# Performance work log

Measured on AMD Instinct MI355X. Metric: run time of the kernel, lower is better.

## Reference

```python
import jax, jax.numpy as jnp
import numpy as np

NEG_INF = -1e30
EPS = 1e-7  # keras.backend.epsilon()

B, T, C, L = 256, 1024, 128, 128


def setup_inputs() -> dict:
    key = jax.random.key(0)
    k1, k2, k3, k4 = jax.random.split(key, 4)
    # ctc_batch_cost expects softmax probabilities in y_pred
    y_pred = jax.nn.softmax(jax.random.normal(k1, (B, T, C), dtype=jnp.float32), axis=-1)
    y_true = jax.random.randint(k2, (B, L), 0, C - 1)           # blank = C-1 excluded from labels
    input_length = jax.random.randint(k3, (B, 1), T // 2, T + 1)
    label_length = jax.random.randint(k4, (B, 1), L // 2, L + 1)
    return {"y_true": y_true, "y_pred": y_pred,
            "input_length": input_length, "label_length": label_length}


def _ctc_batch_cost(y_true, y_pred, input_length, label_length):
    """Faithful jax version of keras.backend.ctc_batch_cost (blank = num_classes-1)."""
    b, t_max, c = y_pred.shape
    l_max = y_true.shape[1]
    s_max = 2 * l_max + 1
    blank = c - 1

    logp = jnp.log(y_pred + EPS)                                # [B,T,C]

    # Extended label sequence: blank, l0, blank, l1, ..., blank  -> [B,S]
    ext = jnp.full((b, s_max), blank, dtype=y_true.dtype)
    ext = ext.at[:, 1::2].set(y_true)

    # Gather log-probs of extended labels per time step -> [B,T,S]
    lp_ext = jnp.take_along_axis(logp, ext[:, None, :], axis=2)

    # Skip transition (s-2 -> s) allowed iff ext[s] != blank and ext[s] != ext[s-2]
    same = jnp.concatenate([jnp.ones((b, 2), bool), ext[:, 2:] == ext[:, :-2]], axis=1)
    skip_ok = (ext != blank) & (~same)                          # [B,S]

    # Valid extended positions given per-sample label_length
    s_idx = jnp.arange(s_max)
    valid_s = s_idx[None, :] < (2 * label_length + 1)           # [B,S]

    ll = label_length[:, 0]
    il = input_length[:, 0]

    alpha0 = jnp.full((b, s_max), NEG_INF, dtype=logp.dtype)
    alpha0 = alpha0.at[:, 0].set(lp_ext[:, 0, 0])
    alpha0 = alpha0.at[:, 1].set(jnp.where(ll > 0, lp_ext[:, 0, 1], NEG_INF))

    neg1 = jnp.full((b, 1), NEG_INF, dtype=logp.dtype)
    neg2 = jnp.full((b, 2), NEG_INF, dtype=logp.dtype)

    def step(alpha, inputs):
        lp_t, t = inputs                                        # lp_t: [B,S]
        a1 = alpha
        a2 = jnp.concatenate([neg1, alpha[:, :-1]], axis=1)
        a3 = jnp.where(skip_ok, jnp.concatenate([neg2, alpha[:, :-2]], axis=1), NEG_INF)
        m = jnp.maximum(jnp.maximum(a1, a2), a3)
        new = m + jnp.log(jnp.exp(a1 - m) + jnp.exp(a2 - m) + jnp.exp(a3 - m)) + lp_t
        new = jnp.where(valid_s, new, NEG_INF)
        alpha = jnp.where((t < il)[:, None], new, alpha)        # freeze past input_length
        return alpha, None

    lp_seq = jnp.moveaxis(lp_ext, 1, 0)[1:]                     # [T-1,B,S]
    ts = jnp.arange(1, t_max)
    alpha_T, _ = jax.lax.scan(step, alpha0, (lp_seq, ts))

    end = 2 * ll                                                # index of final blank
    a_end = jnp.take_along_axis(alpha_T, end[:, None], axis=1)[:, 0]
    a_pen = jnp.take_along_axis(alpha_T, jnp.maximum(end - 1, 0)[:, None], axis=1)[:, 0]
    a_pen = jnp.where(ll > 0, a_pen, NEG_INF)
    loglik = jnp.logaddexp(a_end, a_pen)
    return -loglik[:, None]                                     # [B,1], as ctc_batch_cost


def reference(y_true, y_pred, input_length, label_length):
    # CTCLayer.call computes the loss (add_loss) and returns y_pred; for the
    # kernel baseline we return the loss itself, which is the actual compute.
    return _ctc_batch_cost(y_true, y_pred, input_length, label_length)
```

## Files before the change

kernel.cpp:

```cpp
#include <hip/hip_runtime.h>


constexpr int   Tn    = 1024;
constexpr int   Cc    = 128;
constexpr int   Ln    = 128;
constexpr float EPSf  = 1e-7f;
constexpr int   CK    = 15;
constexpr int   NSLOT = 4;

__device__ __forceinline__ int dpp_max_i32(int m) {
    int o;
    o = __builtin_amdgcn_update_dpp(0, m, 0x111, 0xf, 0xf, false); m = o > m ? o : m;
    o = __builtin_amdgcn_update_dpp(0, m, 0x112, 0xf, 0xf, false); m = o > m ? o : m;
    o = __builtin_amdgcn_update_dpp(0, m, 0x114, 0xf, 0xf, false); m = o > m ? o : m;
    o = __builtin_amdgcn_update_dpp(0, m, 0x118, 0xf, 0xf, false); m = o > m ? o : m;
    o = __builtin_amdgcn_update_dpp(0, m, 0x142, 0xf, 0xf, false); m = o > m ? o : m;
    o = __builtin_amdgcn_update_dpp(0, m, 0x143, 0xf, 0xf, false); m = o > m ? o : m;
    return m;
}

__device__ __forceinline__ double dpp_shr1_f64(double x) {
    const int lo = __double2loint(x), hi = __double2hiint(x);
    const int slo = __builtin_amdgcn_update_dpp(0, lo, 0x138, 0xf, 0xf, true);
    const int shi = __builtin_amdgcn_update_dpp(0, hi, 0x138, 0xf, 0xf, true);
    return __hiloint2double(shi, slo);
}

__global__ __launch_bounds__(128, 1)
void ctc_fwd_kernel(const int*   __restrict__ y_true,
                    const float* __restrict__ y_pred,
                    const int*   __restrict__ in_len,
                    const int*   __restrict__ lab_len,
                    float*       __restrict__ out)
{
    const int tid = threadIdx.x;
    const int L   = tid & 63;
    const int b   = blockIdx.x;
    const int il  = in_len[b];
    const int ll  = lab_len[b];
    const int blank = Cc - 1;

    const int* yb   = y_true + (size_t)b * Ln;
    const int  lab1 = yb[2 * L];
    const int  lab2 = yb[2 * L + 1];

    const float* base = y_pred + (size_t)b * Tn * Cc;
    const int steps = (il > 0) ? (il - 1) : 0;
    const int nfull = steps / CK;
    const int nch   = (steps + CK - 1) / CK;

    __shared__ float  f32L1[NSLOT][CK][64];
    __shared__ float  f32L2[NSLOT][CK][64];
    __shared__ float  f32BK[NSLOT][CK];
    __shared__ double sA[258];

#define BARRIER() do {                                                  \
    __builtin_amdgcn_sched_barrier(0);                                  \
    asm volatile("" ::: "memory");                                      \
    __builtin_amdgcn_s_barrier();                                       \
    asm volatile("" ::: "memory");                                      \
    __builtin_amdgcn_sched_barrier(0);                                  \
} while (0)

#define WAIT_VM(n) do {                                                 \
    __builtin_amdgcn_sched_barrier(0);                                  \
    asm volatile("s_waitcnt vmcnt(" #n ")");                            \
    __builtin_amdgcn_sched_barrier(0);                                  \
} while (0)

    if (tid >= 64) {
#define ISSUE_CHUNK(k) do {                                             \
    const int slot_ = (k) & (NSLOT - 1);                                \
    {                                                                   \
        int tb_ = 1 + (k) * CK + L; if (tb_ > steps) tb_ = steps; if (tb_ < 0) tb_ = 0; \
        const float* g_ = base + (size_t)tb_ * Cc + blank;              \
        if (L < CK)                                                     \
            __builtin_amdgcn_global_load_lds(                           \
                (const __attribute__((address_space(1))) void*)g_,      \
                (__attribute__((address_space(3))) void*)&f32BK[slot_][0], 4, 0, 0); \
    }                                                                   \
    _Pragma("unroll")                                                   \
    for (int r_ = 0; r_ < CK; ++r_) {                                   \
        int t_ = 1 + (k) * CK + r_; if (t_ > steps) t_ = steps; if (t_ < 0) t_ = 0; \
        const float* row_ = base + (size_t)t_ * Cc;                     \
        __builtin_amdgcn_global_load_lds(                               \
            (const __attribute__((address_space(1))) void*)(row_ + lab1), \
            (__attribute__((address_space(3))) void*)&f32L1[slot_][r_][0], 4, 0, 0); \
        __builtin_amdgcn_global_load_lds(                               \
            (const __attribute__((address_space(1))) void*)(row_ + lab2), \
            (__attribute__((address_space(3))) void*)&f32L2[slot_][r_][0], 4, 0, 0); \
    }                                                                   \
} while (0)

        ISSUE_CHUNK(0);
        ISSUE_CHUNK(1);
        WAIT_VM(31);
        BARRIER();
        for (int i = 0; i < nch; ++i) {
            if (i + 2 < nch) {
                ISSUE_CHUNK(i + 2);
                WAIT_VM(31);
            } else {
                WAIT_VM(0);
            }
            BARRIER();
        }
        return;
#undef ISSUE_CHUNK
    }

    const int  labp = (L > 0) ? yb[2 * L - 1] : -1;
    const double skm1 = ((L > 0) && (lab1 != blank) && (lab1 != labp)) ? 1.0 : 0.0;
    const double skm3 = ((lab2 != blank) && (lab2 != lab1)) ? 1.0 : 0.0;

    double a0 = 0.0, a1v = 0.0, a2v = 0.0, a3v = 0.0, a4v = 0.0;
    if (L == 0) {
        a0  = (double)(base[blank] + EPSf);
        a1v = (ll > 0) ? (double)(base[lab1] + EPSf) : 0.0;
    }
    int shift = 0;

#define DPSTEP(qb_, q1_, q2_) do {                                      \
    const double pa3_ = dpp_shr1_f64(a3v);                              \
    const double n0_ = (a0 + pa3_) * (qb_);                             \
    const double n1_ = fma(skm1, pa3_, a0 + a1v) * (q1_);               \
    const double n2_ = (a2v + a1v) * (qb_);                             \
    const double n3_ = fma(skm3, a1v, a3v + a2v) * (q2_);               \
    const double n4_ = (a4v + a3v) * (qb_);                             \
    a0 = n0_; a1v = n1_; a2v = n2_; a3v = n3_; a4v = n4_;               \
} while (0)

#define RESCALE() do {                                                  \
    double m_ = fmax(fmax(a0, a1v), fmax(a2v, a3v)); m_ = fmax(m_, a4v);\
    int be_ = (__double2hiint(m_) >> 20) & 0x7ff;                       \
    be_ = dpp_max_i32(be_);                                             \
    const int emax_ = __builtin_amdgcn_readlane(be_, 63);               \
    const double sc_ = __hiloint2double((2046 - emax_) << 20, 0);       \
    a0 *= sc_; a1v *= sc_; a2v *= sc_; a3v *= sc_; a4v *= sc_;          \
    shift += emax_ - 1023;                                              \
} while (0)

    BARRIER();

    for (int i = 0; i < nch; ++i) {
        const int slot = i & (NSLOT - 1);

        double qb[CK], q1[CK], q2[CK];
#pragma unroll
        for (int r = 0; r < CK; ++r) {
            qb[r] = (double)(f32BK[slot][r]    + EPSf);
            q1[r] = (double)(f32L1[slot][r][L] + EPSf);
            q2[r] = (double)(f32L2[slot][r][L] + EPSf);
        }

        BARRIER();

        if (i < nfull) {
#pragma unroll
            for (int r = 0; r < CK; ++r)
                DPSTEP(qb[r], q1[r], q2[r]);
        } else {
#pragma unroll
            for (int r = 0; r < CK; ++r) {
                if (1 + i * CK + r <= steps)
                    DPSTEP(qb[r], q1[r], q2[r]);
            }
        }
        RESCALE();
    }

    sA[4 * L + 0] = a0;
    sA[4 * L + 1] = a1v;
    sA[4 * L + 2] = a2v;
    sA[4 * L + 3] = a3v;
    if (L == 63) sA[256] = a4v;

    if (L == 0) {
        const int end = 2 * ll;
        const double ae = sA[end];
        int pi = end - 1; if (pi < 0) pi = 0;
        double ap = sA[pi];
        if (ll <= 0) ap = 0.0;
        const double s  = ae + ap;
        const double lg = log2(s) + (double)shift;
        out[b] = (float)(-0.6931471805599453 * lg);
    }

#undef BARRIER
#undef WAIT_VM
#undef DPSTEP
#undef RESCALE
}

extern "C" void kernel_launch(void* const* d_in, const int* in_sizes, int n_in,
                              void* d_out, int out_size, void* d_ws, size_t ws_size,
                              hipStream_t stream) {
    const int*   y_true  = (const int*)  d_in[0];
    const float* y_pred  = (const float*)d_in[1];
    const int*   in_len  = (const int*)  d_in[2];
    const int*   lab_len = (const int*)  d_in[3];
    float*       out     = (float*)      d_out;

    ctc_fwd_kernel<<<dim3(256), dim3(128), 0, stream>>>(y_true, y_pred, in_len, lab_len, out);
}
```

Before: 58.49 us.

## Switch CTC alpha recursion from fp64 to fp32 with per-lane exponent shifts

Replaces the double-precision scaled-probability recursion with fp32, keeping a separate exponent offset for each lane instead of one wave-wide shift. Neighbour contributions are rescaled with ldexp by the clamped difference in lane shifts, and lanes whose values fall too far below their left neighbour are zeroed. The chunk size drops from 15 to 8 time steps, so fewer values are held in registers but rescaling runs more often. This removes slow fp64 arithmetic, at the cost of more complicated rescale logic and possible accuracy loss.

Result: slower. 70.90 us (+21.2%).

```diff
diff --git a/kernel.cpp b/kernel.cpp
--- a/kernel.cpp
+++ b/kernel.cpp
@@ -5,25 +5,15 @@
 constexpr int   Cc    = 128;
 constexpr int   Ln    = 128;
 constexpr float EPSf  = 1e-7f;
-constexpr int   CK    = 15;
+constexpr int   CK    = 8;
 constexpr int   NSLOT = 4;
 
-__device__ __forceinline__ int dpp_max_i32(int m) {
-    int o;
-    o = __builtin_amdgcn_update_dpp(0, m, 0x111, 0xf, 0xf, false); m = o > m ? o : m;
-    o = __builtin_amdgcn_update_dpp(0, m, 0x112, 0xf, 0xf, false); m = o > m ? o : m;
-    o = __builtin_amdgcn_update_dpp(0, m, 0x114, 0xf, 0xf, false); m = o > m ? o : m;
-    o = __builtin_amdgcn_update_dpp(0, m, 0x118, 0xf, 0xf, false); m = o > m ? o : m;
-    o = __builtin_amdgcn_update_dpp(0, m, 0x142, 0xf, 0xf, false); m = o > m ? o : m;
-    o = __builtin_amdgcn_update_dpp(0, m, 0x143, 0xf, 0xf, false); m = o > m ? o : m;
-    return m;
-}
-
-__device__ __forceinline__ double dpp_shr1_f64(double x) {
-    const int lo = __double2loint(x), hi = __double2hiint(x);
-    const int slo = __builtin_amdgcn_update_dpp(0, lo, 0x138, 0xf, 0xf, true);
-    const int shi = __builtin_amdgcn_update_dpp(0, hi, 0x138, 0xf, 0xf, true);
-    return __hiloint2double(shi, slo);
+__device__ __forceinline__ float dpp_shr1_f32(float x) {
+    int s = __builtin_amdgcn_update_dpp(0, __float_as_int(x), 0x138, 0xf, 0xf, true);
+    return __int_as_float(s);
+}
+__device__ __forceinline__ int dpp_shr1_i32(int x) {
+    return __builtin_amdgcn_update_dpp(0, x, 0x138, 0xf, 0xf, true);
 }
 
 __global__ __launch_bounds__(128, 1)
@@ -49,10 +39,11 @@
     const int nfull = steps / CK;
     const int nch   = (steps + CK - 1) / CK;
 
-    __shared__ float  f32L1[NSLOT][CK][64];
-    __shared__ float  f32L2[NSLOT][CK][64];
-    __shared__ float  f32BK[NSLOT][CK];
-    __shared__ double sA[258];
+    __shared__ float f32L1[NSLOT][CK][64];
+    __shared__ float f32L2[NSLOT][CK][64];
+    __shared__ float f32BK[NSLOT][CK];
+    __shared__ float sAf[258];
+    __shared__ int   sShL[64];
 
 #define BARRIER() do {                                                  \
     __builtin_amdgcn_sched_barrier(0);                                  \
@@ -94,12 +85,12 @@
 
         ISSUE_CHUNK(0);
         ISSUE_CHUNK(1);
-        WAIT_VM(31);
+        WAIT_VM(17);
         BARRIER();
         for (int i = 0; i < nch; ++i) {
             if (i + 2 < nch) {
                 ISSUE_CHUNK(i + 2);
-                WAIT_VM(31);
+                WAIT_VM(17);
             } else {
                 WAIT_VM(0);
             }
@@ -109,35 +100,56 @@
 #undef ISSUE_CHUNK
     }
 
-    const int  labp = (L > 0) ? yb[2 * L - 1] : -1;
-    const double skm1 = ((L > 0) && (lab1 != blank) && (lab1 != labp)) ? 1.0 : 0.0;
-    const double skm3 = ((lab2 != blank) && (lab2 != lab1)) ? 1.0 : 0.0;
-
-    double a0 = 0.0, a1v = 0.0, a2v = 0.0, a3v = 0.0, a4v = 0.0;
+    const int  labp  = (L > 0) ? yb[2 * L - 1] : -1;
+    const float skm1 = ((L > 0) && (lab1 != blank) && (lab1 != labp)) ? 1.0f : 0.0f;
+    const float skm3 = ((lab2 != blank) && (lab2 != lab1)) ? 1.0f : 0.0f;
+
+    float a0 = 0.f, a1v = 0.f, a2v = 0.f, a3v = 0.f, a4v = 0.f;
     if (L == 0) {
-        a0  = (double)(base[blank] + EPSf);
-        a1v = (ll > 0) ? (double)(base[lab1] + EPSf) : 0.0;
-    }
-    int shift = 0;
+        a0  = base[blank] + EPSf;
+        a1v = (ll > 0) ? (base[lab1] + EPSf) : 0.f;
+    }
+    int sh = 0;
+    int dl = 0;
 
 #define DPSTEP(qb_, q1_, q2_) do {                                      \
-    const double pa3_ = dpp_shr1_f64(a3v);                              \
-    const double n0_ = (a0 + pa3_) * (qb_);                             \
-    const double n1_ = fma(skm1, pa3_, a0 + a1v) * (q1_);               \
-    const double n2_ = (a2v + a1v) * (qb_);                             \
-    const double n3_ = fma(skm3, a1v, a3v + a2v) * (q2_);               \
-    const double n4_ = (a4v + a3v) * (qb_);                             \
+    const float pa3_ = ldexpf(dpp_shr1_f32(a3v), dl);                   \
+    const float n0_ = (a0 + pa3_) * (qb_);                              \
+    const float n1_ = fmaf(skm1, pa3_, a0 + a1v) * (q1_);               \
+    const float n2_ = (a2v + a1v) * (qb_);                              \
+    const float n3_ = fmaf(skm3, a1v, a3v + a2v) * (q2_);               \
+    const float n4_ = (a4v + a3v) * (qb_);                              \
     a0 = n0_; a1v = n1_; a2v = n2_; a3v = n3_; a4v = n4_;               \
 } while (0)
 
 #define RESCALE() do {                                                  \
-    double m_ = fmax(fmax(a0, a1v), fmax(a2v, a3v)); m_ = fmax(m_, a4v);\
-    int be_ = (__double2hiint(m_) >> 20) & 0x7ff;                       \
-    be_ = dpp_max_i32(be_);                                             \
-    const int emax_ = __builtin_amdgcn_readlane(be_, 63);               \
-    const double sc_ = __hiloint2double((2046 - emax_) << 20, 0);       \
+    float m_ = fmaxf(fmaxf(fmaxf(a0, a1v), fmaxf(a2v, a3v)), a4v);      \
+    const bool occ_ = (m_ > 0.f);                                       \
+    const int  ef_  = (int)((__float_as_uint(m_) >> 23) & 255u);        \
+    const int  eff_ = occ_ ? ef_ : 127;                                 \
+    const int  e_   = eff_ - 127;                                       \
+    const float sc_ = __uint_as_float((unsigned)(254 - eff_) << 23);    \
     a0 *= sc_; a1v *= sc_; a2v *= sc_; a3v *= sc_; a4v *= sc_;          \
-    shift += emax_ - 1023;                                              \
+    const int nsh_ = sh + e_;                                           \
+    const unsigned long long mk_ = __ballot(occ_);                      \
+    const int last_ = mk_ ? (63 - __builtin_clzll(mk_)) : 0;            \
+    const int adopt_ = __builtin_amdgcn_readlane(nsh_, last_);          \
+    sh = occ_ ? nsh_ : adopt_;                                          \
+    bool zf_ = false;                                                   \
+    _Pragma("unroll")                                                   \
+    for (int k_ = 0; k_ < 3; ++k_) {                                    \
+        const int shl_ = dpp_shr1_i32(sh);                              \
+        const int d_   = (L == 0) ? 0 : (shl_ - sh);                    \
+        const bool big_ = (L > 0) && (d_ > 96);                         \
+        sh = big_ ? shl_ : sh;                                          \
+        zf_ = zf_ || big_;                                              \
+    }                                                                   \
+    {                                                                   \
+        const int shl_ = dpp_shr1_i32(sh);                              \
+        int d_ = (L == 0) ? 0 : (shl_ - sh);                            \
+        dl = (d_ > 96) ? 96 : d_;                                       \
+    }                                                                   \
+    if (zf_) { a0 = 0.f; a1v = 0.f; a2v = 0.f; a3v = 0.f; a4v = 0.f; }  \
 } while (0)
 
     BARRIER();
@@ -145,12 +157,12 @@
     for (int i = 0; i < nch; ++i) {
         const int slot = i & (NSLOT - 1);
 
-        double qb[CK], q1[CK], q2[CK];
+        float qb[CK], q1[CK], q2[CK];
 #pragma unroll
         for (int r = 0; r < CK; ++r) {
-            qb[r] = (double)(f32BK[slot][r]    + EPSf);
-            q1[r] = (double)(f32L1[slot][r][L] + EPSf);
-            q2[r] = (double)(f32L2[slot][r][L] + EPSf);
+            qb[r] = f32BK[slot][r]    + EPSf;
+            q1[r] = f32L1[slot][r][L] + EPSf;
+            q2[r] = f32L2[slot][r][L] + EPSf;
         }
 
         BARRIER();
@@ -169,21 +181,28 @@
         RESCALE();
     }
 
-    sA[4 * L + 0] = a0;
-    sA[4 * L + 1] = a1v;
-    sA[4 * L + 2] = a2v;
-    sA[4 * L + 3] = a3v;
-    if (L == 63) sA[256] = a4v;
+    sAf[4 * L + 0] = a0;
+    sAf[4 * L + 1] = a1v;
+    sAf[4 * L + 2] = a2v;
+    sAf[4 * L + 3] = a3v;
+    if (L == 63) sAf[256] = a4v;
+    sShL[L] = sh;
 
     if (L == 0) {
         const int end = 2 * ll;
-        const double ae = sA[end];
         int pi = end - 1; if (pi < 0) pi = 0;
-        double ap = sA[pi];
-        if (ll <= 0) ap = 0.0;
-        const double s  = ae + ap;
-        const double lg = log2(s) + (double)shift;
-        out[b] = (float)(-0.6931471805599453 * lg);
+        const float ve = sAf[end];
+        float vp = sAf[pi];
+        if (ll <= 0) vp = 0.f;
+        int ie = end >> 2; if (ie > 63) ie = 63;
+        int ip = pi  >> 2; if (ip > 63) ip = 63;
+        const int she = sShL[ie];
+        const int shp = sShL[ip];
+        const float le = (ve > 0.f) ? ((float)she + log2f(ve)) : -3.0e38f;
+        const float lp = (vp > 0.f) ? ((float)shp + log2f(vp)) : -3.0e38f;
+        const float mx = fmaxf(le, lp);
+        const float r  = mx + log2f(exp2f(le - mx) + exp2f(lp - mx));
+        out[b] = -0.69314718055994530942f * r;
     }
 
 #undef BARRIER
```
